# Kernel tuning notes

Measured on AMD Instinct MI355X. Metric: run time of the kernel, lower is better.

## Reference

```python
import jax, jax.numpy as jnp
import numpy as np

NUM_EXPERTS = 8
TOP_K = 2
ROUTE_SCALE = 1.0
DIM = 1024
HID = 1024
B, S = 2, 4096


def setup_inputs() -> dict:
    key = jax.random.key(0)
    ks = jax.random.split(key, 9)
    sc = 0.05
    return {
        "x": jax.random.normal(ks[0], (B, S, DIM), dtype=jnp.float32),
        "gate_w": jax.random.normal(ks[1], (NUM_EXPERTS, DIM), dtype=jnp.float32) * sc,
        "w1": jax.random.normal(ks[2], (NUM_EXPERTS, HID, DIM), dtype=jnp.float32) * sc,
        "w2": jax.random.normal(ks[3], (NUM_EXPERTS, DIM, HID), dtype=jnp.float32) * sc,
        "w3": jax.random.normal(ks[4], (NUM_EXPERTS, HID, DIM), dtype=jnp.float32) * sc,
        "sw1": jax.random.normal(ks[5], (HID, DIM), dtype=jnp.float32) * sc,
        "sw2": jax.random.normal(ks[6], (DIM, HID), dtype=jnp.float32) * sc,
        "sw3": jax.random.normal(ks[7], (HID, DIM), dtype=jnp.float32) * sc,
        "expert_bias": jnp.zeros((NUM_EXPERTS,), dtype=jnp.float32),
    }


def reference(x, gate_w, w1, w2, w3, sw1, sw2, sw3, expert_bias):
    bs, slen, dim = x.shape
    xf = x.reshape(-1, dim)                      # [T, D]

    # ---- router (sigmoid scoring, top-k over scores + bias, gather true scores) ----
    scores = jax.nn.sigmoid((xf @ gate_w.T).astype(jnp.float32))   # [T, E]
    _, sel = jax.lax.top_k(scores + expert_bias[None, :], TOP_K)    # [T, K] int32
    top_scores = jnp.take_along_axis(scores, sel, axis=1) * ROUTE_SCALE  # [T, K]

    # ---- stable sort token-slots by chosen expert (dispatch permutation) ----
    flat_sel = sel.reshape(-1)                       # [T*K]
    order = jnp.argsort(flat_sel, stable=True)       # [T*K]
    scores_sorted = top_scores.reshape(-1)[order]    # [T*K]
    tok_idx = order // TOP_K                         # source token per slot
    expert_ids = flat_sel[order]                     # sorted expert id per slot

    routed = xf[tok_idx]                             # gather [T*K, D]
    # score_before_experts=True: scale inputs by routing score
    routed = (routed.astype(jnp.float32) * scores_sorted[:, None]).astype(x.dtype)

    # ---- grouped expert GLU MLP (loop over fixed expert count, masked) ----
    out_r = jnp.zeros_like(routed)
    for e in range(NUM_EXPERTS):
        m = (expert_ids == e)[:, None]
        h = jax.nn.silu(routed @ w1[e].T) * (routed @ w3[e].T)   # [T*K, H]
        out_r = out_r + jnp.where(m, h @ w2[e].T, jnp.zeros((), routed.dtype))

    # ---- shared expert on all tokens ----
    shared = (jax.nn.silu(xf @ sw1.T) * (xf @ sw3.T)) @ sw2.T    # [T, D]

    # NOTE: original code multiplies by routing scores again after experts
    # (in addition to score_before_experts) -- replicated faithfully.
    out_r = (out_r.astype(jnp.float32) * scores_sorted[:, None]).astype(x.dtype)

    out = shared.at[tok_idx].add(out_r)              # scatter-add combine
    return out.reshape(bs, slen, dim)
```

## Files before the change

### kernel.cpp

```cpp
#include <hip/hip_runtime.h>
#include <stdint.h>

typedef unsigned short u16;
typedef unsigned int u32;

#define T_TOK 8192
#define DIMSZ 1024
#define HIDSZ 1024
#define NE 8
#define NSLOT (T_TOK * 2)
#define NPAD (NSLOT + 1024)

typedef __attribute__((ext_vector_type(8))) __bf16 bf16x8;
typedef __attribute__((ext_vector_type(16))) float f32x16;

#define MFMA32(a, b, c) __builtin_amdgcn_mfma_f32_32x32x16_bf16(a, b, c, 0, 0, 0)

__device__ __forceinline__ size_t ablk(int pos, int c) {
  return ((((size_t)(pos >> 7) * 32 + (c >> 5)) * 4 + ((c >> 3) & 3)) * 128 +
          (pos & 127)) * 8 + (c & 7);
}

__device__ __forceinline__ u16 f2bf(float f) {
  u32 u = __builtin_bit_cast(u32, f);
  u += 0x7FFFu + ((u >> 16) & 1u);
  return (u16)(u >> 16);
}
__device__ __forceinline__ float bflo(u32 v) { return __builtin_bit_cast(float, v << 16); }
__device__ __forceinline__ float bfhi(u32 v) { return __builtin_bit_cast(float, v & 0xffff0000u); }
__device__ __forceinline__ u32 pack2(float a, float b) {
  return (u32)f2bf(a) | ((u32)f2bf(b) << 16);
}
__device__ __forceinline__ float silu_f(float v) { return v / (1.f + expf(-v)); }

__device__ __forceinline__ void gload16(const void* g, void* l) {
  __builtin_amdgcn_global_load_lds(
      (const __attribute__((address_space(1))) unsigned int*)g,
      (__attribute__((address_space(3))) unsigned int*)l, 16, 0, 0);
}

#define PIPE_SYNC(N) asm volatile("s_waitcnt vmcnt(" #N ")\n\ts_barrier" ::: "memory")

__global__ __launch_bounds__(256) void convert_blocked(
    const float* __restrict__ s0, const float* __restrict__ s1,
    const float* __restrict__ s2, const float* __restrict__ ss0,
    const float* __restrict__ ss1, const float* __restrict__ ss2,
    u16* __restrict__ d0, u16* __restrict__ d1, u16* __restrict__ d2,
    u16* __restrict__ ds0, u16* __restrict__ ds1, u16* __restrict__ ds2) {
  __shared__ u16 lt[2048];
  int t = blockIdx.x;
  const float* s;
  u16* d;
  if (t < NE * 16 * 32) {
    s = (blockIdx.y == 0) ? s0 : (blockIdx.y == 1) ? s1 : s2;
    d = (blockIdx.y == 0) ? d0 : (blockIdx.y == 1) ? d1 : d2;
  } else {
    t -= NE * 16 * 32;
    s = (blockIdx.y == 0) ? ss0 : (blockIdx.y == 1) ? ss1 : ss2;
    d = (blockIdx.y == 0) ? ds0 : (blockIdx.y == 1) ? ds1 : ds2;
  }
  int rt = t >> 5, kt = t & 31;
  const float* sp = s + (size_t)rt * 64 * 1024 + kt * 32;
  int nl = threadIdx.x >> 2, k0 = (threadIdx.x & 3) * 8;
  float4 a = *(const float4*)(sp + (size_t)nl * 1024 + k0);
  float4 b = *(const float4*)(sp + (size_t)nl * 1024 + k0 + 4);
  uint4 p;
  p.x = pack2(a.x, a.y); p.y = pack2(a.z, a.w);
  p.z = pack2(b.x, b.y); p.w = pack2(b.z, b.w);
  *(uint4*)&lt[(threadIdx.x & 3) * 512 + nl * 8] = p;
  __syncthreads();
  *(uint4*)(d + (size_t)t * 2048 + threadIdx.x * 8) = *(const uint4*)&lt[threadIdx.x * 8];
}

__global__ __launch_bounds__(256) void router_kernel(
    const float* __restrict__ x, const float* __restrict__ gw,
    const float* __restrict__ bias, int* __restrict__ sel,
    float* __restrict__ selscore, u16* __restrict__ xb) {
  int t = blockIdx.x * 4 + (threadIdx.x >> 6);
  int lane = threadIdx.x & 63;
  float a[NE];
#pragma unroll
  for (int e = 0; e < NE; e++) a[e] = 0.f;
#pragma unroll
  for (int j = 0; j < 4; j++) {
    int c = j * 256 + lane * 4;
    float4 xv = *(const float4*)&x[(size_t)t * DIMSZ + c];
    uint2 p;
    p.x = pack2(xv.x, xv.y);
    p.y = pack2(xv.z, xv.w);
    *(uint2*)&xb[ablk(t, c)] = p;
#pragma unroll
    for (int e = 0; e < NE; e++) {
      float4 gv = *(const float4*)&gw[e * DIMSZ + c];
      a[e] = fmaf(xv.x, gv.x, fmaf(xv.y, gv.y, fmaf(xv.z, gv.z, fmaf(xv.w, gv.w, a[e]))));
    }
  }
#pragma unroll
  for (int off = 1; off < 64; off <<= 1)
#pragma unroll
    for (int e = 0; e < NE; e++) a[e] += __shfl_xor(a[e], off);
  if (lane == 0) {
    float s[NE], b[NE];
#pragma unroll
    for (int e = 0; e < NE; e++) {
      s[e] = 1.f / (1.f + expf(-a[e]));
      b[e] = s[e] + bias[e];
    }
    int e1 = 0; float v1 = b[0];
#pragma unroll
    for (int e = 1; e < NE; e++) if (b[e] > v1) { v1 = b[e]; e1 = e; }
    int e2 = -1; float v2 = -1e30f;
#pragma unroll
    for (int e = 0; e < NE; e++) if (e != e1 && b[e] > v2) { v2 = b[e]; e2 = e; }
    sel[t * 2] = e1; sel[t * 2 + 1] = e2;
    selscore[t * 2] = s[e1];
    selscore[t * 2 + 1] = s[e2];
  }
}

__global__ __launch_bounds__(1024) void rank_kernel(
    const int* __restrict__ sel, const float* __restrict__ selscore,
    int* __restrict__ slot2pos, float* __restrict__ slot_score,
    int* __restrict__ counts, int* __restrict__ offsets) {
  __shared__ int hist[NE * 1024];
  __shared__ int tot[NE];
  __shared__ int offs[NE];
  int tid = threadIdx.x;
  int sl[16];
  int h[NE];
#pragma unroll
  for (int e = 0; e < NE; e++) h[e] = 0;
#pragma unroll
  for (int j = 0; j < 4; j++) {
    int4 v = ((const int4*)sel)[tid * 4 + j];
    sl[j * 4 + 0] = v.x; sl[j * 4 + 1] = v.y;
    sl[j * 4 + 2] = v.z; sl[j * 4 + 3] = v.w;
  }
#pragma unroll
  for (int i = 0; i < 16; i++)
#pragma unroll
    for (int e = 0; e < NE; e++) h[e] += (sl[i] == e) ? 1 : 0;
#pragma unroll
  for (int e = 0; e < NE; e++) hist[e * 1024 + tid] = h[e];
  __syncthreads();
  int wid = tid >> 6, lane = tid & 63;
  if (wid < NE) {
    int e = wid;
    int vals[16];
    int lsum = 0;
#pragma unroll
    for (int i = 0; i < 16; i++) {
      int v = hist[e * 1024 + lane * 16 + i];
      vals[i] = lsum;
      lsum += v;
    }
    int incl = lsum;
#pragma unroll
    for (int off = 1; off < 64; off <<= 1) {
      int v = __shfl_up(incl, off);
      if (lane >= off) incl += v;
    }
    int excl = incl - lsum;
#pragma unroll
    for (int i = 0; i < 16; i++) hist[e * 1024 + lane * 16 + i] = vals[i] + excl;
    if (lane == 63) tot[e] = incl;
  }
  __syncthreads();
  if (tid == 0) {
    int acc = 0;
    for (int e = 0; e < NE; e++) {
      offs[e] = acc;
      offsets[e] = acc;
      counts[e] = tot[e];
      acc += (tot[e] + 127) & ~127;
    }
  }
  __syncthreads();
  int base[NE];
#pragma unroll
  for (int e = 0; e < NE; e++) base[e] = offs[e] + hist[e * 1024 + tid];
#pragma unroll
  for (int i = 0; i < 16; i++) {
    int slot = tid * 16 + i;
    int e = sl[i];
    int pos = 0;
#pragma unroll
    for (int k = 0; k < NE; k++) pos += (e == k) ? base[k] : 0;
#pragma unroll
    for (int k = 0; k < NE; k++) base[k] += (e == k) ? 1 : 0;
    slot2pos[slot] = pos;
    slot_score[pos] = selscore[slot];
  }
}

__global__ __launch_bounds__(256) void gather_kernel(
    const u16* __restrict__ xb, const float* __restrict__ selscore,
    const int* __restrict__ slot2pos, u16* __restrict__ routed) {
  int s = blockIdx.x * 4 + (threadIdx.x >> 6);
  int lane = threadIdx.x & 63;
  int pos = slot2pos[s];
  float sc = selscore[s];
  int t = s >> 1;
#pragma unroll
  for (int j = 0; j < 4; j++) {
    int c = j * 256 + lane * 4;
    uint2 v = *(const uint2*)&xb[ablk(t, c)];
    uint2 p;
    p.x = pack2(bflo(v.x) * sc, bfhi(v.x) * sc);
    p.y = pack2(bflo(v.y) * sc, bfhi(v.y) * sc);
    *(uint2*)&routed[ablk(pos, c)] = p;
  }
}


#define BUFE 12288

#define PIPE_STAGE(B, KT, pA, pB0, pB1)                        \
  do {                                                         \
    u16* Lb = &lds[(B) * BUFE];                                \
    const u16* a_ = (pA) + (size_t)(KT) * 4096;                \
    gload16(a_, Lb + tid * 8);                                 \
    gload16(a_ + 2048, Lb + 2048 + tid * 8);                   \
    gload16(a_ + 32 * 4096, Lb + 4096 + tid * 8);              \
    gload16(a_ + 32 * 4096 + 2048, Lb + 6144 + tid * 8);       \
    gload16((pB0) + (size_t)(KT) * 2048, Lb + 8192 + tid * 8); \
    gload16((pB1) + (size_t)(KT) * 2048, Lb + 10240 + tid * 8);\
  } while (0)

#define PIPE_COMPUTE(B)                                             \
  do {                                                              \
    const u16* La = &lds[(B) * BUFE] + wy * 4096;                   \
    const u16* Lw = &lds[(B) * BUFE] + 8192 + wx * 2048;            \
    _Pragma("unroll")                                               \
    for (int s = 0; s < 2; s++) {                                   \
      int kc = 2 * s + l5;                                          \
      bf16x8 b0 = *(const bf16x8*)&Lw[(kc * 64 + l31) * 8];         \
      bf16x8 b1 = *(const bf16x8*)&Lw[(kc * 64 + 32 + l31) * 8];    \
      _Pragma("unroll")                                             \
      for (int i = 0; i < 4; i++) {                                 \
        bf16x8 a = *(const bf16x8*)&La[(kc * 128 + i * 32 + l31) * 8]; \
        acc[i][0] = MFMA32(a, b0, acc[i][0]);                       \
        acc[i][1] = MFMA32(a, b1, acc[i][1]);                       \
      }                                                             \
    }                                                               \
  } while (0)

#define PIPE_LOOP(pA, pB0, pB1)                 \
  PIPE_STAGE(0, 0, pA, pB0, pB1);               \
  PIPE_STAGE(1, 1, pA, pB0, pB1);               \
  {                                             \
    int c0 = 0, c1 = 1, c2 = 2;                 \
    for (int kt = 0; kt < 31; ++kt) {           \
      PIPE_SYNC(6);                             \
      if (kt < 30) PIPE_STAGE(c2, kt + 2, pA, pB0, pB1); \
      PIPE_COMPUTE(c0);                         \
      int tmp = c0; c0 = c1; c1 = c2; c2 = tmp; \
    }                                           \
    PIPE_SYNC(0);                               \
    PIPE_COMPUTE(c0);                           \
  }

__global__ __launch_bounds__(256, 2) void dual_glu_gemm(
    const u16* __restrict__ A, const u16* __restrict__ W1,
    const u16* __restrict__ W3, u16* __restrict__ Hout,
    const u16* __restrict__ As, const u16* __restrict__ SW1,
    const u16* __restrict__ SW3, u16* __restrict__ Hs,
    const int* __restrict__ seg_off, const int* __restrict__ seg_cnt) {
  int z = blockIdx.z;
  const u16 *Ap, *w1p, *w3p;
  u16* Hp;
  int soff, scnt;
  if (z < NE) {
    soff = seg_off[z]; scnt = seg_cnt[z];
    Ap = A;
    w1p = W1 + (size_t)z * HIDSZ * DIMSZ;
    w3p = W3 + (size_t)z * HIDSZ * DIMSZ;
    Hp = Hout;
  } else {
    soff = 0; scnt = T_TOK;
    Ap = As; w1p = SW1; w3p = SW3;
    Hp = Hs;
  }
  int mbase = blockIdx.y * 256;
  if (mbase >= scnt) return;
  int hx = blockIdx.x;

  __shared__ u16 lds[3 * BUFE];

  int tid = threadIdx.x;
  int lane = tid & 63;
  int wid = tid >> 6;
  int wy = wid >> 1, wx = wid & 1;
  int l5 = lane >> 5, l31 = lane & 31;

  const u16* pA = Ap + ((size_t)((soff + mbase) >> 7) * 32) * 4096 + tid * 8;
  const u16* pB1 = w1p + ((size_t)hx * 32) * 2048 + tid * 8;
  const u16* pB3 = w3p + ((size_t)hx * 32) * 2048 + tid * 8;

  f32x16 acc[4][2];
#pragma unroll
  for (int i = 0; i < 4; i++) { acc[i][0] = (f32x16)0.f; acc[i][1] = (f32x16)0.f; }

  PIPE_LOOP(pA, pB1, pB3);

  __syncthreads();
  float* ex = (float*)lds;
  if (wx == 0) {
#pragma unroll
    for (int i = 0; i < 4; i++)
#pragma unroll
      for (int j = 0; j < 2; j++)
#pragma unroll
        for (int r = 0; r < 16; r++) {
          int row = wy * 128 + i * 32 + (r & 3) + 8 * (r >> 2) + 4 * l5;
          ex[row * 64 + j * 32 + l31] = acc[i][j][r];
        }
  }
  __syncthreads();
  if (wx == 1) {
#pragma unroll
    for (int i = 0; i < 4; i++)
#pragma unroll
      for (int j = 0; j < 2; j++)
#pragma unroll
        for (int r = 0; r < 16; r++) {
          int row = wy * 128 + i * 32 + (r & 3) + 8 * (r >> 2) + 4 * l5;
          int grow = mbase + row;
          if (grow < scnt) {
            float h1 = ex[row * 64 + j * 32 + l31];
            Hp[ablk(soff + grow, hx * 64 + j * 32 + l31)] =
                f2bf(silu_f(h1) * acc[i][j][r]);
          }
        }
  }
}

__global__ __launch_bounds__(256, 2) void gemm2_kernel(
    const u16* __restrict__ A, const u16* __restrict__ W, u16* __restrict__ OutB,
    const u16* __restrict__ As, const u16* __restrict__ SW, float* __restrict__ OutF,
    const float* __restrict__ scale, const int* __restrict__ seg_off,
    const int* __restrict__ seg_cnt) {
  int z = blockIdx.z;
  const u16 *Ap, *wp;
  int soff, scnt;
  if (z < NE) {
    soff = seg_off[z]; scnt = seg_cnt[z];
    Ap = A; wp = W + (size_t)z * DIMSZ * HIDSZ;
  } else {
    soff = 0; scnt = T_TOK;
    Ap = As; wp = SW;
  }
  int mbase = blockIdx.y * 256;
  if (mbase >= scnt) return;
  int nbase = blockIdx.x * 128;

  __shared__ u16 lds[3 * BUFE];

  int tid = threadIdx.x;
  int lane = tid & 63;
  int wid = tid >> 6;
  int wy = wid >> 1, wx = wid & 1;
  int l5 = lane >> 5, l31 = lane & 31;

  const u16* pA = Ap + ((size_t)((soff + mbase) >> 7) * 32) * 4096 + tid * 8;
  const u16* pB0 = wp + ((size_t)(nbase >> 6) * 32) * 2048 + tid * 8;
  const u16* pB1 = pB0 + (size_t)32 * 2048;

  f32x16 acc[4][2];
#pragma unroll
  for (int i = 0; i < 4; i++) { acc[i][0] = (f32x16)0.f; acc[i][1] = (f32x16)0.f; }

  PIPE_LOOP(pA, pB0, pB1);

#pragma unroll
  for (int i = 0; i < 4; i++)
#pragma unroll
    for (int j = 0; j < 2; j++) {
      int colg = nbase + wx * 64 + j * 32 + l31;
#pragma unroll
      for (int r = 0; r < 16; r++) {
        int rowl = (r & 3) + 8 * (r >> 2) + 4 * l5;
        int grow = mbase + wy * 128 + i * 32 + rowl;
        if (grow < scnt) {
          size_t idx = (size_t)(soff + grow) * DIMSZ + colg;
          if (z < NE) {
            OutB[idx] = f2bf(acc[i][j][r] * scale[soff + grow]);
          } else {
            OutF[idx] = acc[i][j][r];
          }
        }
      }
    }
}

__global__ __launch_bounds__(256) void combine_kernel(
    float* __restrict__ out, const u16* __restrict__ Orb,
    const int* __restrict__ slot2pos) {
  int t = blockIdx.x;
  int d = threadIdx.x * 4;
  int p0 = slot2pos[t * 2];
  int p1 = slot2pos[t * 2 + 1];
  float4 o = *(float4*)&out[(size_t)t * DIMSZ + d];
  uint2 a = *(const uint2*)&Orb[(size_t)p0 * DIMSZ + d];
  uint2 b = *(const uint2*)&Orb[(size_t)p1 * DIMSZ + d];
  o.x += bflo(a.x) + bflo(b.x);
  o.y += bfhi(a.x) + bfhi(b.x);
  o.z += bflo(a.y) + bflo(b.y);
  o.w += bfhi(a.y) + bfhi(b.y);
  *(float4*)&out[(size_t)t * DIMSZ + d] = o;
}

extern "C" void kernel_launch(void* const* d_in, const int* in_sizes, int n_in,
                              void* d_out, int out_size, void* d_ws, size_t ws_size,
                              hipStream_t stream) {
  const float* x = (const float*)d_in[0];
  const float* gw = (const float*)d_in[1];
  const float* w1 = (const float*)d_in[2];
  const float* w2 = (const float*)d_in[3];
  const float* w3 = (const float*)d_in[4];
  const float* sw1 = (const float*)d_in[5];
  const float* sw2 = (const float*)d_in[6];
  const float* sw3 = (const float*)d_in[7];
  const float* bias = (const float*)d_in[8];
  float* out = (float*)d_out;

  uint8_t* ws = (uint8_t*)d_ws;
  size_t off = 0;
  auto alloc = [&](size_t b) { size_t o = off; off += (b + 255) & ~(size_t)255; return o; };

  size_t ctrl = alloc(256);
  int* counts = (int*)(ws + ctrl);
  int* offsets = counts + 16;
  int* sel = (int*)(ws + alloc((size_t)NSLOT * 4));
  float* selscore = (float*)(ws + alloc((size_t)NSLOT * 4));
  float* slot_score = (float*)(ws + alloc((size_t)NPAD * 4));
  int* slot2pos = (int*)(ws + alloc((size_t)NSLOT * 4));
  u16* xb = (u16*)(ws + alloc((size_t)T_TOK * DIMSZ * 2));
  u16* routed = (u16*)(ws + alloc((size_t)NPAD * DIMSZ * 2));
  u16* Hbuf = (u16*)(ws + alloc((size_t)NPAD * HIDSZ * 2));
  u16* Orb = (u16*)(ws + alloc((size_t)NPAD * DIMSZ * 2));
  u16* Hs = (u16*)(ws + alloc((size_t)T_TOK * HIDSZ * 2));
  u16* w1b = (u16*)(ws + alloc((size_t)NE * HIDSZ * DIMSZ * 2));
  u16* w2b = (u16*)(ws + alloc((size_t)NE * DIMSZ * HIDSZ * 2));
  u16* w3b = (u16*)(ws + alloc((size_t)NE * HIDSZ * DIMSZ * 2));
  u16* sw1b = (u16*)(ws + alloc((size_t)HIDSZ * DIMSZ * 2));
  u16* sw2b = (u16*)(ws + alloc((size_t)DIMSZ * HIDSZ * 2));
  u16* sw3b = (u16*)(ws + alloc((size_t)HIDSZ * DIMSZ * 2));

  convert_blocked<<<dim3((NE + 1) * 16 * 32, 3), 256, 0, stream>>>(
      w1, w2, w3, sw1, sw2, sw3, w1b, w2b, w3b, sw1b, sw2b, sw3b);

  router_kernel<<<T_TOK / 4, 256, 0, stream>>>(x, gw, bias, sel, selscore, xb);
  rank_kernel<<<1, 1024, 0, stream>>>(sel, selscore, slot2pos, slot_score,
                                      counts, offsets);
  gather_kernel<<<NSLOT / 4, 256, 0, stream>>>(xb, selscore, slot2pos, routed);

  dual_glu_gemm<<<dim3(16, 32, NE + 1), 256, 0, stream>>>(
      routed, w1b, w3b, Hbuf, xb, sw1b, sw3b, Hs, offsets, counts);
  gemm2_kernel<<<dim3(8, 32, NE + 1), 256, 0, stream>>>(
      Hbuf, w2b, Orb, Hs, sw2b, out, slot_score, offsets, counts);

  combine_kernel<<<T_TOK, 256, 0, stream>>>(out, Orb, slot2pos);
}
```

Baseline: 534.2 us.

## Shrink GEMM tiles to 128x128 with 8 waves and prioritize MFMA issue

Both grouped GEMM kernels go from 256x128 tiles with 4 waves to 128x128 tiles with 8 waves (512 threads), each wave holding 2 accumulator blocks instead of 8. The LDS stage shrinks, and the pipeline loop now waits on fewer outstanding loads. s_setprio is raised around the MFMA sections. The aim is more blocks per CU and less padding waste on ragged expert segments, in exchange for less operand reuse per block and more LDS and global traffic per FLOP.

```diff
diff --git a/kernel.cpp b/kernel.cpp
--- a/kernel.cpp
+++ b/kernel.cpp
@@ -212,55 +212,54 @@
   }
 }
 
-
-#define BUFE 12288
-
-#define PIPE_STAGE(B, KT, pA, pB0, pB1)                        \
-  do {                                                         \
-    u16* Lb = &lds[(B) * BUFE];                                \
-    const u16* a_ = (pA) + (size_t)(KT) * 4096;                \
-    gload16(a_, Lb + tid * 8);                                 \
-    gload16(a_ + 2048, Lb + 2048 + tid * 8);                   \
-    gload16(a_ + 32 * 4096, Lb + 4096 + tid * 8);              \
-    gload16(a_ + 32 * 4096 + 2048, Lb + 6144 + tid * 8);       \
-    gload16((pB0) + (size_t)(KT) * 2048, Lb + 8192 + tid * 8); \
-    gload16((pB1) + (size_t)(KT) * 2048, Lb + 10240 + tid * 8);\
+#define BUFE 8192
+
+#define PIPE_STAGE(B, KT)                                         \
+  do {                                                            \
+    u16* Lb = &lds[(B) * BUFE];                                   \
+    gload16(pA + (size_t)(KT) * 4096, Lb + tid * 8);              \
+    gload16(pBm + (size_t)(KT) * 2048, Lb + bdst);                \
   } while (0)
 
-#define PIPE_COMPUTE(B)                                             \
-  do {                                                              \
-    const u16* La = &lds[(B) * BUFE] + wy * 4096;                   \
-    const u16* Lw = &lds[(B) * BUFE] + 8192 + wx * 2048;            \
-    _Pragma("unroll")                                               \
-    for (int s = 0; s < 2; s++) {                                   \
-      int kc = 2 * s + l5;                                          \
-      bf16x8 b0 = *(const bf16x8*)&Lw[(kc * 64 + l31) * 8];         \
-      bf16x8 b1 = *(const bf16x8*)&Lw[(kc * 64 + 32 + l31) * 8];    \
-      _Pragma("unroll")                                             \
-      for (int i = 0; i < 4; i++) {                                 \
-        bf16x8 a = *(const bf16x8*)&La[(kc * 128 + i * 32 + l31) * 8]; \
-        acc[i][0] = MFMA32(a, b0, acc[i][0]);                       \
-        acc[i][1] = MFMA32(a, b1, acc[i][1]);                       \
-      }                                                             \
-    }                                                               \
+#define PIPE_COMPUTE(B)                                               \
+  do {                                                                \
+    const u16* Lb = &lds[(B) * BUFE];                                 \
+    _Pragma("unroll")                                                 \
+    for (int c = 0; c < 2; c++) {                                     \
+      int ko = 2 * c + l5;                                            \
+      bf16x8 b = *(const bf16x8*)&Lb[4096 + bsel + ko * 512 + l31 * 8]; \
+      bf16x8 a0 = *(const bf16x8*)&Lb[ko * 1024 + wy * 512 + l31 * 8];  \
+      bf16x8 a1 = *(const bf16x8*)&Lb[ko * 1024 + wy * 512 + 256 + l31 * 8]; \
+      acc[0] = MFMA32(a0, b, acc[0]);                                 \
+      acc[1] = MFMA32(a1, b, acc[1]);                                 \
+    }                                                                 \
   } while (0)
 
-#define PIPE_LOOP(pA, pB0, pB1)                 \
-  PIPE_STAGE(0, 0, pA, pB0, pB1);               \
-  PIPE_STAGE(1, 1, pA, pB0, pB1);               \
-  {                                             \
-    int c0 = 0, c1 = 1, c2 = 2;                 \
-    for (int kt = 0; kt < 31; ++kt) {           \
-      PIPE_SYNC(6);                             \
-      if (kt < 30) PIPE_STAGE(c2, kt + 2, pA, pB0, pB1); \
-      PIPE_COMPUTE(c0);                         \
-      int tmp = c0; c0 = c1; c1 = c2; c2 = tmp; \
-    }                                           \
-    PIPE_SYNC(0);                               \
-    PIPE_COMPUTE(c0);                           \
-  }
-
-__global__ __launch_bounds__(256, 2) void dual_glu_gemm(
+#define PIPE_LOOP()                                                   \
+  PIPE_STAGE(0, 0);                                                   \
+  PIPE_STAGE(1, 1);                                                   \
+  {                                                                   \
+    int c0 = 0, c1 = 1, c2 = 2;                                       \
+    for (int t = 0; t < 30; ++t) {                                    \
+      PIPE_SYNC(2);                                                   \
+      PIPE_STAGE(c2, t + 2);                                          \
+      __builtin_amdgcn_s_setprio(1);                                  \
+      PIPE_COMPUTE(c0);                                               \
+      __builtin_amdgcn_s_setprio(0);                                  \
+      int tm = c0; c0 = c1; c1 = c2; c2 = tm;                         \
+    }                                                                 \
+    PIPE_SYNC(2);                                                     \
+    __builtin_amdgcn_s_setprio(1);                                    \
+    PIPE_COMPUTE(c0);                                                 \
+    __builtin_amdgcn_s_setprio(0);                                    \
+    c0 = c1;                                                          \
+    PIPE_SYNC(0);                                                     \
+    __builtin_amdgcn_s_setprio(1);                                    \
+    PIPE_COMPUTE(c0);                                                 \
+    __builtin_amdgcn_s_setprio(0);                                    \
+  }
+
+__global__ __launch_bounds__(512, 4) void dual_glu_gemm(
     const u16* __restrict__ A, const u16* __restrict__ W1,
     const u16* __restrict__ W3, u16* __restrict__ Hout,
     const u16* __restrict__ As, const u16* __restrict__ SW1,
@@ -281,7 +280,7 @@
     Ap = As; w1p = SW1; w3p = SW3;
     Hp = Hs;
   }
-  int mbase = blockIdx.y * 256;
+  int mbase = blockIdx.y * 128;
   if (mbase >= scnt) return;
   int hx = blockIdx.x;
 
@@ -290,52 +289,51 @@
   int tid = threadIdx.x;
   int lane = tid & 63;
   int wid = tid >> 6;
-  int wy = wid >> 1, wx = wid & 1;
+  int wy = wid >> 2, wq = wid & 3;
   int l5 = lane >> 5, l31 = lane & 31;
 
-  const u16* pA = Ap + ((size_t)((soff + mbase) >> 7) * 32) * 4096 + tid * 8;
-  const u16* pB1 = w1p + ((size_t)hx * 32) * 2048 + tid * 8;
-  const u16* pB3 = w3p + ((size_t)hx * 32) * 2048 + tid * 8;
-
-  f32x16 acc[4][2];
-#pragma unroll
-  for (int i = 0; i < 4; i++) { acc[i][0] = (f32x16)0.f; acc[i][1] = (f32x16)0.f; }
-
-  PIPE_LOOP(pA, pB1, pB3);
+  const u16* pA = Ap + (size_t)((soff + mbase) >> 7) * 32 * 4096 + tid * 8;
+  const u16* w1u = w1p + (size_t)hx * 32 * 2048;
+  const u16* w3u = w3p + (size_t)hx * 32 * 2048;
+  const u16* pBm = ((tid >> 8) ? w3u : w1u) + (tid & 255) * 8;
+  int bdst = 4096 + (tid >> 8) * 2048 + (tid & 255) * 8;
+  int bsel = (wq >> 1) * 2048 + (wq & 1) * 256;
+
+  f32x16 acc[2];
+  acc[0] = (f32x16)0.f; acc[1] = (f32x16)0.f;
+
+  PIPE_LOOP();
 
   __syncthreads();
   float* ex = (float*)lds;
-  if (wx == 0) {
-#pragma unroll
-    for (int i = 0; i < 4; i++)
-#pragma unroll
-      for (int j = 0; j < 2; j++)
-#pragma unroll
-        for (int r = 0; r < 16; r++) {
-          int row = wy * 128 + i * 32 + (r & 3) + 8 * (r >> 2) + 4 * l5;
-          ex[row * 64 + j * 32 + l31] = acc[i][j][r];
+  int region = wy * 2 + (wq & 1);
+  if (wq < 2) {
+#pragma unroll
+    for (int i = 0; i < 2; i++)
+#pragma unroll
+      for (int r = 0; r < 16; r++) {
+        int rowl = (r & 3) + 8 * (r >> 2) + 4 * l5;
+        ex[region * 2048 + (i * 32 + rowl) * 32 + l31] = acc[i][r];
+      }
+  }
+  __syncthreads();
+  if (wq >= 2) {
+#pragma unroll
+    for (int i = 0; i < 2; i++)
+#pragma unroll
+      for (int r = 0; r < 16; r++) {
+        int rowl = (r & 3) + 8 * (r >> 2) + 4 * l5;
+        int grow = mbase + wy * 64 + i * 32 + rowl;
+        if (grow < scnt) {
+          float h1 = ex[region * 2048 + (i * 32 + rowl) * 32 + l31];
+          Hp[ablk(soff + grow, hx * 64 + (wq & 1) * 32 + l31)] =
+              f2bf(silu_f(h1) * acc[i][r]);
         }
-  }
-  __syncthreads();
-  if (wx == 1) {
-#pragma unroll
-    for (int i = 0; i < 4; i++)
-#pragma unroll
-      for (int j = 0; j < 2; j++)
-#pragma unroll
-        for (int r = 0; r < 16; r++) {
-          int row = wy * 128 + i * 32 + (r & 3) + 8 * (r >> 2) + 4 * l5;
-          int grow = mbase + row;
-          if (grow < scnt) {
-            float h1 = ex[row * 64 + j * 32 + l31];
-            Hp[ablk(soff + grow, hx * 64 + j * 32 + l31)] =
-                f2bf(silu_f(h1) * acc[i][j][r]);
-          }
-        }
-  }
-}
-
-__global__ __launch_bounds__(256, 2) void gemm2_kernel(
+      }
+  }
+}
+
+__global__ __launch_bounds__(512, 4) void gemm2_kernel(
     const u16* __restrict__ A, const u16* __restrict__ W, u16* __restrict__ OutB,
     const u16* __restrict__ As, const u16* __restrict__ SW, float* __restrict__ OutF,
     const float* __restrict__ scale, const int* __restrict__ seg_off,
@@ -350,7 +348,7 @@
     soff = 0; scnt = T_TOK;
     Ap = As; wp = SW;
   }
-  int mbase = blockIdx.y * 256;
+  int mbase = blockIdx.y * 128;
   if (mbase >= scnt) return;
   int nbase = blockIdx.x * 128;
 
@@ -359,38 +357,37 @@
   int tid = threadIdx.x;
   int lane = tid & 63;
   int wid = tid >> 6;
-  int wy = wid >> 1, wx = wid & 1;
+  int wy = wid >> 2, wq = wid & 3;
   int l5 = lane >> 5, l31 = lane & 31;
 
-  const u16* pA = Ap + ((size_t)((soff + mbase) >> 7) * 32) * 4096 + tid * 8;
-  const u16* pB0 = wp + ((size_t)(nbase >> 6) * 32) * 2048 + tid * 8;
-  const u16* pB1 = pB0 + (size_t)32 * 2048;
-
-  f32x16 acc[4][2];
-#pragma unroll
-  for (int i = 0; i < 4; i++) { acc[i][0] = (f32x16)0.f; acc[i][1] = (f32x16)0.f; }
-
-  PIPE_LOOP(pA, pB0, pB1);
-
-#pragma unroll
-  for (int i = 0; i < 4; i++)
-#pragma unroll
-    for (int j = 0; j < 2; j++) {
-      int colg = nbase + wx * 64 + j * 32 + l31;
-#pragma unroll
-      for (int r = 0; r < 16; r++) {
-        int rowl = (r & 3) + 8 * (r >> 2) + 4 * l5;
-        int grow = mbase + wy * 128 + i * 32 + rowl;
-        if (grow < scnt) {
-          size_t idx = (size_t)(soff + grow) * DIMSZ + colg;
-          if (z < NE) {
-            OutB[idx] = f2bf(acc[i][j][r] * scale[soff + grow]);
-          } else {
-            OutF[idx] = acc[i][j][r];
-          }
+  const u16* pA = Ap + (size_t)((soff + mbase) >> 7) * 32 * 4096 + tid * 8;
+  const u16* nt0 = wp + (size_t)(nbase >> 6) * 32 * 2048;
+  const u16* pBm = nt0 + (size_t)(tid >> 8) * 32 * 2048 + (tid & 255) * 8;
+  int bdst = 4096 + (tid >> 8) * 2048 + (tid & 255) * 8;
+  int bsel = (wq >> 1) * 2048 + (wq & 1) * 256;
+
+  f32x16 acc[2];
+  acc[0] = (f32x16)0.f; acc[1] = (f32x16)0.f;
+
+  PIPE_LOOP();
+
+#pragma unroll
+  for (int i = 0; i < 2; i++) {
+    int colg = nbase + wq * 32 + l31;
+#pragma unroll
+    for (int r = 0; r < 16; r++) {
+      int rowl = (r & 3) + 8 * (r >> 2) + 4 * l5;
+      int grow = mbase + wy * 64 + i * 32 + rowl;
+      if (grow < scnt) {
+        size_t idx = (size_t)(soff + grow) * DIMSZ + colg;
+        if (z < NE) {
+          OutB[idx] = f2bf(acc[i][r] * scale[soff + grow]);
+        } else {
+          OutF[idx] = acc[i][r];
         }
       }
     }
+  }
 }
 
 __global__ __launch_bounds__(256) void combine_kernel(
@@ -455,9 +452,9 @@
                                       counts, offsets);
   gather_kernel<<<NSLOT / 4, 256, 0, stream>>>(xb, selscore, slot2pos, routed);
 
-  dual_glu_gemm<<<dim3(16, 32, NE + 1), 256, 0, stream>>>(
+  dual_glu_gemm<<<dim3(16, 64, NE + 1), 512, 0, stream>>>(
       routed, w1b, w3b, Hbuf, xb, sw1b, sw3b, Hs, offsets, counts);
-  gemm2_kernel<<<dim3(8, 32, NE + 1), 256, 0, stream>>>(
+  gemm2_kernel<<<dim3(8, 64, NE + 1), 512, 0, stream>>>(
       Hbuf, w2b, Orb, Hs, sw2b, out, slot_score, offsets, counts);
 
   combine_kernel<<<T_TOK, 256, 0, stream>>>(out, Orb, slot2pos);
```

Result: faster. 495.0 us (-7.3%).
